# Kernel tuning notes

Measured on AMD Instinct MI355X. Metric: run time of the kernel, lower is better.

The kernel has to match this reference:

```python
import jax, jax.numpy as jnp
import numpy as np

B, S, D, H = 2, 2048, 2048, 16
HD = D // H  # 128


def setup_inputs() -> dict:
    key = jax.random.key(0)
    ks = jax.random.split(key, 5)
    scale = 0.02
    return {
        "hidden_states": jax.random.normal(ks[0], (B, S, D), dtype=jnp.float32),
        "Wqkv_w": jax.random.normal(ks[1], (3 * D, D), dtype=jnp.float32) * scale,
        "Wqkv_b": jax.random.normal(ks[2], (3 * D,), dtype=jnp.float32) * scale,
        "out_w": jax.random.normal(ks[3], (D, D), dtype=jnp.float32) * scale,
        "out_b": jax.random.normal(ks[4], (D,), dtype=jnp.float32) * scale,
    }


def reference(hidden_states, Wqkv_w, Wqkv_b, out_w, out_b):
    b, s, d = hidden_states.shape
    # QKV projection (torch Linear: x @ W.T + b)
    qkv = hidden_states @ Wqkv_w.T + Wqkv_b          # [b, s, 3d]
    qkv = qkv.reshape(b, s, 3, H, HD)                 # 'b s (three h d)'
    q, k, v = qkv[:, :, 0], qkv[:, :, 1], qkv[:, :, 2]  # [b, s, h, hd]
    softmax_scale = 1.0 / np.float32(np.sqrt(HD))
    # full quadratic scores, matching the naive baddbmm path
    scores = jnp.einsum('bthd,bshd->bhts', q, k) * softmax_scale  # [b,h,t,s]
    # causal=False (module default), dropout_p=0.0 -> no mask, no dropout
    attn = jax.nn.softmax(scores, axis=-1)
    ctx = jnp.einsum('bhts,bshd->bthd', attn, v)      # [b, t, h, hd]
    ctx = ctx.reshape(b, s, d)
    return ctx @ out_w.T + out_b
```

## Files before the change

### kernel.cpp

```cpp
#include <hip/hip_runtime.h>
#include <cstdint>
#include <cstddef>

#define B_ 2
#define S_ 2048
#define D_ 2048
#define H_ 16
#define HD_ 128
#define NTOK 4096
#define NQKV 6144

typedef unsigned short u16;
typedef __attribute__((ext_vector_type(8))) __bf16 bf16x8;
typedef __attribute__((ext_vector_type(4))) float f32x4;

__device__ __forceinline__ u16 f2bf(float f) {
  uint32_t u = __builtin_bit_cast(uint32_t, f);
  u = (u + 0x7FFFu + ((u >> 16) & 1u)) >> 16;
  return (u16)u;
}

__device__ __forceinline__ void gload_lds16(const void* g, void* l) {
  __builtin_amdgcn_global_load_lds(
      (const __attribute__((address_space(1))) void*)g,
      (__attribute__((address_space(3))) void*)l, 16, 0, 0);
}

__global__ void cvt_all(const float* __restrict__ hs, const float* __restrict__ wqkv,
                        const float* __restrict__ wo,
                        u16* __restrict__ hsb, u16* __restrict__ wqkvb,
                        u16* __restrict__ wob) {
  const int n1 = (B_ * S_ * D_) / 8;
  const int n2 = n1 + (NQKV * D_) / 8;
  const int n3 = n2 + (D_ * D_) / 8;
  int idx = blockIdx.x * blockDim.x + threadIdx.x;
  int stride = gridDim.x * blockDim.x;
  for (int i = idx; i < n3; i += stride) {
    const float* src; u16* dst; int j;
    if (i < n1)      { src = hs;   dst = hsb;   j = i; }
    else if (i < n2) { src = wqkv; dst = wqkvb; j = i - n1; }
    else             { src = wo;   dst = wob;   j = i - n2; }
    const float4* s = (const float4*)(src + (size_t)j * 8);
    float4 a = s[0], b = s[1];
    union { u16 u[8]; uint4 v; } o;
    o.u[0] = f2bf(a.x); o.u[1] = f2bf(a.y); o.u[2] = f2bf(a.z); o.u[3] = f2bf(a.w);
    o.u[4] = f2bf(b.x); o.u[5] = f2bf(b.y); o.u[6] = f2bf(b.z); o.u[7] = f2bf(b.w);
    *(uint4*)(dst + (size_t)j * 8) = o.v;
  }
}


#define PH_MID() do { asm volatile("s_barrier" ::: "memory"); \
  __builtin_amdgcn_s_setprio(1); } while (0)
#define PH_END() do { __builtin_amdgcn_s_setprio(0); \
  asm volatile("s_barrier" ::: "memory"); } while (0)
#define PH_END_VM(n) do { __builtin_amdgcn_s_setprio(0); \
  asm volatile("s_waitcnt vmcnt(" #n ")" ::: "memory"); \
  asm volatile("s_barrier" ::: "memory"); } while (0)

#define STA(sl,buf,ko) gload_lds16(aSrc + (size_t)(sl)*64*D_ + (ko), aDst + (buf)*16384 + (sl)*4096)
#define STB(sl,buf,ko) gload_lds16(bSrc + (size_t)(sl)*64*D_ + (ko), bDst + (buf)*12288 + (sl)*4096)

#define LOADB(buf) do { _Pragma("unroll") for (int nf = 0; nf < 3; ++nf) \
  _Pragma("unroll") for (int kk = 0; kk < 2; ++kk) \
    breg[nf][kk] = *(const bf16x8*)(sB + (buf)*12288 + (wn*48 + nf*16 + fr)*64 + ((((kk<<2)|fq)^swz)<<3)); } while (0)
#define LOADA_A(buf,q) do { _Pragma("unroll") for (int mm = 0; mm < 2; ++mm) \
  _Pragma("unroll") for (int kk = 0; kk < 2; ++kk) \
    arA[mm][kk] = *(const bf16x8*)(sA + (buf)*16384 + (wm*128 + ((q)*2+mm)*16 + fr)*64 + ((((kk<<2)|fq)^swz)<<3)); } while (0)
#define LOADA_B(buf,q) do { _Pragma("unroll") for (int mm = 0; mm < 2; ++mm) \
  _Pragma("unroll") for (int kk = 0; kk < 2; ++kk) \
    arB[mm][kk] = *(const bf16x8*)(sA + (buf)*16384 + (wm*128 + ((q)*2+mm)*16 + fr)*64 + ((((kk<<2)|fq)^swz)<<3)); } while (0)
#define MFMA12_A(q) do { _Pragma("unroll") for (int kk = 0; kk < 2; ++kk) \
  _Pragma("unroll") for (int mm = 0; mm < 2; ++mm) \
  _Pragma("unroll") for (int nf = 0; nf < 3; ++nf) \
    acc[(q)*2+mm][nf] = __builtin_amdgcn_mfma_f32_16x16x32_bf16(arA[mm][kk], breg[nf][kk], acc[(q)*2+mm][nf], 0, 0, 0); } while (0)
#define MFMA12_B(q) do { _Pragma("unroll") for (int kk = 0; kk < 2; ++kk) \
  _Pragma("unroll") for (int mm = 0; mm < 2; ++mm) \
  _Pragma("unroll") for (int nf = 0; nf < 3; ++nf) \
    acc[(q)*2+mm][nf] = __builtin_amdgcn_mfma_f32_16x16x32_bf16(arB[mm][kk], breg[nf][kk], acc[(q)*2+mm][nf], 0, 0, 0); } while (0)

__global__ __launch_bounds__(512, 2) void qkv_gemm(
    const u16* __restrict__ hsb, const u16* __restrict__ wb,
    const float* __restrict__ bias,
    u16* __restrict__ qb, u16* __restrict__ kb, u16* __restrict__ vT)
{
  __shared__ alignas(1024) u16 sA[2 * 16384];
  __shared__ alignas(1024) u16 sB[2 * 12288];
  const int tid = threadIdx.x;
  const int lane = tid & 63, wid = tid >> 6;
  const int wm = wid >> 2, wn = wid & 3;
  const int fr = lane & 15, fq = lane >> 4;
  const int swz = fr & 7;
  const int m0 = blockIdx.x * 256, n0 = blockIdx.y * 192;

  const int r8 = tid >> 3, g8 = (tid & 7) ^ (r8 & 7);
  const u16* aSrc = hsb + (size_t)(m0 + r8) * D_ + g8 * 8;
  const u16* bSrc = wb  + (size_t)(n0 + r8) * D_ + g8 * 8;
  u16* aDst = sA + wid * 512;
  u16* bDst = sB + wid * 512;

  f32x4 acc[8][3];
  f32x4 z = {0.f, 0.f, 0.f, 0.f};
#pragma unroll
  for (int m = 0; m < 8; ++m)
#pragma unroll
    for (int n = 0; n < 3; ++n) acc[m][n] = z;

  bf16x8 breg[3][2], arA[2][2], arB[2][2];

  STB(0,0,0); STB(1,0,0); STB(2,0,0); STA(0,0,0); STA(1,0,0); STA(2,0,0); STA(3,0,0);
  STB(0,1,64); STB(1,1,64); STB(2,1,64); STA(0,1,64); STA(2,1,64);
  asm volatile("s_waitcnt vmcnt(5)" ::: "memory");
  asm volatile("s_barrier" ::: "memory");

  const int NI = D_ / 128;
#pragma unroll 1
  for (int j = 0; j < NI - 1; ++j) {
    const int kS = (2*j + 1) * 64;
    const int kA = (2*j + 2) * 64;
    const int kB = (2*j + 3) * 64;
    LOADB(0); LOADA_A(0,0); LOADA_B(0,1); STA(1,1,kS); STA(3,1,kS); PH_MID(); MFMA12_A(0); PH_END();
    LOADA_A(0,2);                         STB(0,0,kA); STB(1,0,kA); PH_MID(); MFMA12_B(1); PH_END();
    LOADA_B(0,3);                         STB(2,0,kA); STA(0,0,kA); PH_MID(); MFMA12_A(2); PH_END();
                                          STA(2,0,kA);              PH_MID(); MFMA12_B(3); PH_END_VM(5);
    LOADB(1); LOADA_A(1,0); LOADA_B(1,1); STA(1,0,kA); STA(3,0,kA); PH_MID(); MFMA12_A(0); PH_END();
    LOADA_A(1,2);                         STB(0,1,kB); STB(1,1,kB); PH_MID(); MFMA12_B(1); PH_END();
    LOADA_B(1,3);                         STB(2,1,kB); STA(0,1,kB); PH_MID(); MFMA12_A(2); PH_END();
                                          STA(2,1,kB);              PH_MID(); MFMA12_B(3); PH_END_VM(5);
  }
  {
    const int kS = (2*NI - 1) * 64;
    LOADB(0); LOADA_A(0,0); LOADA_B(0,1); STA(1,1,kS); STA(3,1,kS); PH_MID(); MFMA12_A(0); PH_END();
    LOADA_A(0,2);                                                   PH_MID(); MFMA12_B(1); PH_END();
    LOADA_B(0,3);                                                   PH_MID(); MFMA12_A(2); PH_END();
                                                                    PH_MID(); MFMA12_B(3); PH_END_VM(0);
    LOADB(1); LOADA_A(1,0); LOADA_B(1,1);                           PH_MID(); MFMA12_A(0); PH_END();
    LOADA_A(1,2);                                                   PH_MID(); MFMA12_B(1); PH_END();
    LOADA_B(1,3);                                                   PH_MID(); MFMA12_A(2); PH_END();
                                                                    PH_MID(); MFMA12_B(3); PH_END();
  }

  const float qscale = 0.08838834764831845f;
#pragma unroll
  for (int mf = 0; mf < 8; ++mf)
#pragma unroll
    for (int nf = 0; nf < 3; ++nf) {
      int col = n0 + wn * 48 + nf * 16 + fr;
      float bv = bias[col];
      int t = col >> 11;
      int d2 = col & 2047;
      int h = d2 >> 7, hd = d2 & 127;
#pragma unroll
      for (int r = 0; r < 4; ++r) {
        int row = m0 + wm * 128 + mf * 16 + fq * 4 + r;
        int bb = row >> 11, s = row & 2047;
        int bh = bb * H_ + h;
        float val = acc[mf][nf][r] + bv;
        if (t == 0)      qb[((size_t)bh * S_ + s) * HD_ + hd] = f2bf(val * qscale);
        else if (t == 1) kb[((size_t)bh * S_ + s) * HD_ + hd] = f2bf(val);
        else             vT[((size_t)bh * HD_ + hd) * S_ + s] = f2bf(val);
      }
    }
}

__device__ __forceinline__ void gemm_bt_tile(
    const u16* __restrict__ A, const u16* __restrict__ B,
    int lda, int ldb, int K, int m0, int n0,
    u16* As, u16* Bs, f32x4 acc[4][4])
{
  const int tid = threadIdx.x;
  const int lane = tid & 63;
  const int wid = tid >> 6;
  const int wr = wid >> 1, wc = wid & 1;
  const int fr = lane & 15, fq = lane >> 4;

  for (int k0 = 0; k0 < K; k0 += 32) {
    __syncthreads();
#pragma unroll
    for (int i = 0; i < 2; ++i) {
      int cbase = (i * 4 + wid) * 64;
      int c = cbase + lane;
      int r = c >> 2, c8 = (c & 3) * 8;
      gload_lds16(A + (size_t)(m0 + r) * lda + k0 + c8, As + (size_t)cbase * 8);
      gload_lds16(B + (size_t)(n0 + r) * ldb + k0 + c8, Bs + (size_t)cbase * 8);
    }
    __syncthreads();

    bf16x8 a[4], b[4];
#pragma unroll
    for (int m = 0; m < 4; ++m)
      a[m] = *(const bf16x8*)&As[(wr * 64 + m * 16 + fr) * 32 + fq * 8];
#pragma unroll
    for (int n = 0; n < 4; ++n)
      b[n] = *(const bf16x8*)&Bs[(wc * 64 + n * 16 + fr) * 32 + fq * 8];
#pragma unroll
    for (int m = 0; m < 4; ++m)
#pragma unroll
      for (int n = 0; n < 4; ++n)
        acc[m][n] = __builtin_amdgcn_mfma_f32_16x16x32_bf16(a[m], b[n], acc[m][n], 0, 0, 0);
  }
}

__global__ __launch_bounds__(256) void out_gemm(
    const u16* __restrict__ ctx, const u16* __restrict__ wo,
    const float* __restrict__ bias, float* __restrict__ out)
{
  __shared__ alignas(16) u16 As[128 * 32];
  __shared__ alignas(16) u16 Bs[128 * 32];
  f32x4 acc[4][4];
  f32x4 z = {0.f, 0.f, 0.f, 0.f};
#pragma unroll
  for (int m = 0; m < 4; ++m)
#pragma unroll
    for (int n = 0; n < 4; ++n) acc[m][n] = z;

  int m0 = blockIdx.x * 128, n0 = blockIdx.y * 128;
  gemm_bt_tile(ctx, wo, D_, D_, D_, m0, n0, As, Bs, acc);

  const int lane = threadIdx.x & 63;
  const int wid = threadIdx.x >> 6;
  const int wr = wid >> 1, wc = wid & 1;
  const int fr = lane & 15, fq = lane >> 4;
#pragma unroll
  for (int m = 0; m < 4; ++m)
#pragma unroll
    for (int n = 0; n < 4; ++n) {
      int col = n0 + wc * 64 + n * 16 + fr;
      float bv = bias[col];
#pragma unroll
      for (int r = 0; r < 4; ++r) {
        int row = m0 + wr * 64 + m * 16 + fq * 4 + r;
        out[(size_t)row * D_ + col] = acc[m][n][r] + bv;
      }
    }
}

#define STAGEKV(kvv, buf) do { _Pragma("unroll") \
  for (int i = 0; i < 4; ++i) { \
    int lk = i * 256 + tid; int rk = lk >> 4, sk = lk & 15; \
    gload_lds16(Kg + (size_t)((kvv) + rk) * HD_ + ((sk ^ (rk & 7)) << 3), \
                &Kl[buf][i * 2048 + wid * 512]); \
    int rv = lk >> 3, sv = lk & 7; \
    gload_lds16(Vg + (size_t)rv * S_ + (kvv) + ((sv ^ (rv & 7)) << 3), \
                &Vl[buf][i * 2048 + wid * 512]); \
  } } while (0)

__global__ __launch_bounds__(256, 2) void attn(
    const u16* __restrict__ qb, const u16* __restrict__ kb,
    const u16* __restrict__ vT, u16* __restrict__ ctx)
{
  __shared__ alignas(1024) u16 Kl[2][64 * 128];
  __shared__ alignas(1024) u16 Vl[2][128 * 64];
  __shared__ alignas(16) u16 Pl[4][32 * 64];

  const int tid = threadIdx.x, lane = tid & 63, wid = tid >> 6;
  const int fr = lane & 15, fq = lane >> 4;
  const int bh = blockIdx.y;
  const int q0 = blockIdx.x * 128 + wid * 32;
  f32x4 z = {0.f, 0.f, 0.f, 0.f};

  const u16* Kg = kb + (size_t)bh * S_ * HD_;
  const u16* Vg = vT + (size_t)bh * HD_ * S_;

  STAGEKV(0, 0);

  const u16* qbase = qb + ((size_t)bh * S_ + q0) * HD_;
  bf16x8 qa[2][4];
#pragma unroll
  for (int h = 0; h < 2; ++h)
#pragma unroll
    for (int kc = 0; kc < 4; ++kc)
      qa[h][kc] = *(const bf16x8*)(qbase + (size_t)(h * 16 + fr) * HD_ + kc * 32 + fq * 8);

  f32x4 accv[2][8];
#pragma unroll
  for (int h = 0; h < 2; ++h)
#pragma unroll
    for (int n = 0; n < 8; ++n) accv[h][n] = z;
  float m_run[2] = {-1e30f, -1e30f};
  float l_run[2] = {0.f, 0.f};

  __syncthreads();
  int cur = 0;

  for (int kv = 0; kv < S_; kv += 64) {
    if (kv + 64 < S_) STAGEKV(kv + 64, cur ^ 1);

    const u16* Kc = Kl[cur];
    const u16* Vc = Vl[cur];

    f32x4 sc[2][4];
    __builtin_amdgcn_s_setprio(1);
#pragma unroll
    for (int j = 0; j < 4; ++j) {
      f32x4 s0 = z, s1 = z;
#pragma unroll
      for (int kc = 0; kc < 4; ++kc) {
        int row = j * 16 + fr;
        bf16x8 kf = *(const bf16x8*)&Kc[row * 128 + ((kc * 32 + fq * 8) ^ ((row & 7) << 3))];
        s0 = __builtin_amdgcn_mfma_f32_16x16x32_bf16(kf, qa[0][kc], s0, 0, 0, 0);
        s1 = __builtin_amdgcn_mfma_f32_16x16x32_bf16(kf, qa[1][kc], s1, 0, 0, 0);
      }
      sc[0][j] = s0; sc[1][j] = s1;
    }
    __builtin_amdgcn_s_setprio(0);

    float pmax[2];
#pragma unroll
    for (int h = 0; h < 2; ++h) {
      float mx = sc[h][0][0];
#pragma unroll
      for (int j = 0; j < 4; ++j)
#pragma unroll
        for (int r = 0; r < 4; ++r) mx = fmaxf(mx, sc[h][j][r]);
      mx = fmaxf(mx, __shfl_xor(mx, 16));
      mx = fmaxf(mx, __shfl_xor(mx, 32));
      pmax[h] = mx;
    }

    int need = (pmax[0] > m_run[0] + 8.f) || (pmax[1] > m_run[1] + 8.f);
    if (__any(need)) {
#pragma unroll
      for (int h = 0; h < 2; ++h) {
        float mn = fmaxf(m_run[h], pmax[h]);
        float corr = __expf(m_run[h] - mn);
        m_run[h] = mn;
        l_run[h] *= corr;
#pragma unroll
        for (int r = 0; r < 4; ++r) {
          float rc = __shfl(corr, (lane & 48) | (fq * 4 + r));
#pragma unroll
          for (int n = 0; n < 8; ++n) accv[h][n][r] *= rc;
        }
      }
    }

    u16* Pw = Pl[wid];
#pragma unroll
    for (int h = 0; h < 2; ++h) {
      float ls = 0.f;
#pragma unroll
      for (int j = 0; j < 4; ++j) {
        union { u16 u[4]; ushort4 v; } pk;
#pragma unroll
        for (int r = 0; r < 4; ++r) {
          float p = __expf(sc[h][j][r] - m_run[h]);
          ls += p;
          pk.u[r] = f2bf(p);
        }
        int prow = h * 16 + fr;
        *(ushort4*)&Pw[prow * 64 + ((j * 16 + fq * 4) ^ ((fr & 7) << 3))] = pk.v;
      }
      ls += __shfl_xor(ls, 16);
      ls += __shfl_xor(ls, 32);
      l_run[h] += ls;
    }

    __builtin_amdgcn_s_setprio(1);
#pragma unroll
    for (int kc = 0; kc < 2; ++kc) {
      int pcol = (kc * 32 + fq * 8) ^ ((fr & 7) << 3);
      bf16x8 pa0 = *(const bf16x8*)&Pw[fr * 64 + pcol];
      bf16x8 pa1 = *(const bf16x8*)&Pw[(16 + fr) * 64 + pcol];
#pragma unroll
      for (int n = 0; n < 8; ++n) {
        int row = n * 16 + fr;
        bf16x8 vf = *(const bf16x8*)&Vc[row * 64 + ((kc * 32 + fq * 8) ^ ((row & 7) << 3))];
        accv[0][n] = __builtin_amdgcn_mfma_f32_16x16x32_bf16(pa0, vf, accv[0][n], 0, 0, 0);
        accv[1][n] = __builtin_amdgcn_mfma_f32_16x16x32_bf16(pa1, vf, accv[1][n], 0, 0, 0);
      }
    }
    __builtin_amdgcn_s_setprio(0);

    __syncthreads();
    cur ^= 1;
  }

  float inv[2][4];
#pragma unroll
  for (int h = 0; h < 2; ++h)
#pragma unroll
    for (int r = 0; r < 4; ++r) {
      float l = __shfl(l_run[h], (lane & 48) | (fq * 4 + r));
      inv[h][r] = 1.f / l;
    }
  u16* cb = ctx + (((size_t)(bh >> 4)) * S_ + q0) * D_ + (size_t)(bh & 15) * HD_;
#pragma unroll
  for (int h = 0; h < 2; ++h)
#pragma unroll
    for (int n = 0; n < 8; ++n)
#pragma unroll
      for (int r = 0; r < 4; ++r) {
        int q = h * 16 + fq * 4 + r;
        cb[(size_t)q * D_ + n * 16 + fr] = f2bf(accv[h][n][r] * inv[h][r]);
      }
}

extern "C" void kernel_launch(void* const* d_in, const int* in_sizes, int n_in,
                              void* d_out, int out_size, void* d_ws, size_t ws_size,
                              hipStream_t stream) {
  const float* hs   = (const float*)d_in[0];
  const float* wqkv = (const float*)d_in[1];
  const float* bqkv = (const float*)d_in[2];
  const float* wo   = (const float*)d_in[3];
  const float* bo   = (const float*)d_in[4];
  float* out = (float*)d_out;

  char* ws = (char*)d_ws;
  u16* hsb   = (u16*)(ws);
  u16* wqkvb = (u16*)(ws + 16777216);
  u16* wob   = (u16*)(ws + 41943040);
  u16* qb    = (u16*)(ws + 50331648);
  u16* kb    = (u16*)(ws + 67108864);
  u16* vT    = (u16*)(ws + 83886080);
  u16* ctx   = (u16*)(ws + 100663296);

  cvt_all<<<2048, 256, 0, stream>>>(hs, wqkv, wo, hsb, wqkvb, wob);

  qkv_gemm<<<dim3(NTOK / 256, NQKV / 192), 512, 0, stream>>>(hsb, wqkvb, bqkv, qb, kb, vT);
  attn<<<dim3(S_ / 128, B_ * H_), 256, 0, stream>>>(qb, kb, vT, ctx);
  out_gemm<<<dim3(NTOK / 128, D_ / 128), 256, 0, stream>>>(ctx, wob, bo, out);
}
```

Baseline: 292.8 us.

## Halve QKV GEMM M-tile to 128 rows and restructure pipeline for higher occupancy

The QKV projection GEMM tile shrinks from 256x192 to 128x192. That halves A-tile LDS and the accumulator registers, doubles the grid and raises the launch-bounds occupancy hint from 2 to 4 blocks per CU. The software-pipelined K loop is rewritten to four phases per iteration with new prefetch ordering and waitcnt values. The intent is more blocks in flight and better CU coverage (32x32 = 1024 blocks instead of 512), at the cost of lower arithmetic intensity per loaded B tile and more global traffic.

```diff
diff --git a/kernel.cpp b/kernel.cpp
--- a/kernel.cpp
+++ b/kernel.cpp
@@ -58,7 +58,7 @@
   asm volatile("s_waitcnt vmcnt(" #n ")" ::: "memory"); \
   asm volatile("s_barrier" ::: "memory"); } while (0)
 
-#define STA(sl,buf,ko) gload_lds16(aSrc + (size_t)(sl)*64*D_ + (ko), aDst + (buf)*16384 + (sl)*4096)
+#define STA(sl,buf,ko) gload_lds16(aSrc + (size_t)(sl)*64*D_ + (ko), aDst + (buf)*8192  + (sl)*4096)
 #define STB(sl,buf,ko) gload_lds16(bSrc + (size_t)(sl)*64*D_ + (ko), bDst + (buf)*12288 + (sl)*4096)
 
 #define LOADB(buf) do { _Pragma("unroll") for (int nf = 0; nf < 3; ++nf) \
@@ -66,10 +66,10 @@
     breg[nf][kk] = *(const bf16x8*)(sB + (buf)*12288 + (wn*48 + nf*16 + fr)*64 + ((((kk<<2)|fq)^swz)<<3)); } while (0)
 #define LOADA_A(buf,q) do { _Pragma("unroll") for (int mm = 0; mm < 2; ++mm) \
   _Pragma("unroll") for (int kk = 0; kk < 2; ++kk) \
-    arA[mm][kk] = *(const bf16x8*)(sA + (buf)*16384 + (wm*128 + ((q)*2+mm)*16 + fr)*64 + ((((kk<<2)|fq)^swz)<<3)); } while (0)
+    arA[mm][kk] = *(const bf16x8*)(sA + (buf)*8192 + (wm*64 + ((q)*2+mm)*16 + fr)*64 + ((((kk<<2)|fq)^swz)<<3)); } while (0)
 #define LOADA_B(buf,q) do { _Pragma("unroll") for (int mm = 0; mm < 2; ++mm) \
   _Pragma("unroll") for (int kk = 0; kk < 2; ++kk) \
-    arB[mm][kk] = *(const bf16x8*)(sA + (buf)*16384 + (wm*128 + ((q)*2+mm)*16 + fr)*64 + ((((kk<<2)|fq)^swz)<<3)); } while (0)
+    arB[mm][kk] = *(const bf16x8*)(sA + (buf)*8192 + (wm*64 + ((q)*2+mm)*16 + fr)*64 + ((((kk<<2)|fq)^swz)<<3)); } while (0)
 #define MFMA12_A(q) do { _Pragma("unroll") for (int kk = 0; kk < 2; ++kk) \
   _Pragma("unroll") for (int mm = 0; mm < 2; ++mm) \
   _Pragma("unroll") for (int nf = 0; nf < 3; ++nf) \
@@ -79,19 +79,19 @@
   _Pragma("unroll") for (int nf = 0; nf < 3; ++nf) \
     acc[(q)*2+mm][nf] = __builtin_amdgcn_mfma_f32_16x16x32_bf16(arB[mm][kk], breg[nf][kk], acc[(q)*2+mm][nf], 0, 0, 0); } while (0)
 
-__global__ __launch_bounds__(512, 2) void qkv_gemm(
+__global__ __launch_bounds__(512, 4) void qkv_gemm(
     const u16* __restrict__ hsb, const u16* __restrict__ wb,
     const float* __restrict__ bias,
     u16* __restrict__ qb, u16* __restrict__ kb, u16* __restrict__ vT)
 {
-  __shared__ alignas(1024) u16 sA[2 * 16384];
+  __shared__ alignas(1024) u16 sA[2 * 8192];
   __shared__ alignas(1024) u16 sB[2 * 12288];
   const int tid = threadIdx.x;
   const int lane = tid & 63, wid = tid >> 6;
   const int wm = wid >> 2, wn = wid & 3;
   const int fr = lane & 15, fq = lane >> 4;
   const int swz = fr & 7;
-  const int m0 = blockIdx.x * 256, n0 = blockIdx.y * 192;
+  const int m0 = blockIdx.x * 128, n0 = blockIdx.y * 192;
 
   const int r8 = tid >> 3, g8 = (tid & 7) ^ (r8 & 7);
   const u16* aSrc = hsb + (size_t)(m0 + r8) * D_ + g8 * 8;
@@ -99,50 +99,47 @@
   u16* aDst = sA + wid * 512;
   u16* bDst = sB + wid * 512;
 
-  f32x4 acc[8][3];
+  f32x4 acc[4][3];
   f32x4 z = {0.f, 0.f, 0.f, 0.f};
 #pragma unroll
-  for (int m = 0; m < 8; ++m)
+  for (int m = 0; m < 4; ++m)
 #pragma unroll
     for (int n = 0; n < 3; ++n) acc[m][n] = z;
 
   bf16x8 breg[3][2], arA[2][2], arB[2][2];
 
-  STB(0,0,0); STB(1,0,0); STB(2,0,0); STA(0,0,0); STA(1,0,0); STA(2,0,0); STA(3,0,0);
-  STB(0,1,64); STB(1,1,64); STB(2,1,64); STA(0,1,64); STA(2,1,64);
-  asm volatile("s_waitcnt vmcnt(5)" ::: "memory");
+  STB(0,0,0); STB(1,0,0); STB(2,0,0); STA(0,0,0); STA(1,0,0);
+  STB(0,1,64); STB(1,1,64); STB(2,1,64);
+  asm volatile("s_waitcnt vmcnt(3)" ::: "memory");
   asm volatile("s_barrier" ::: "memory");
 
-  const int NI = D_ / 128;
 #pragma unroll 1
-  for (int j = 0; j < NI - 1; ++j) {
-    const int kS = (2*j + 1) * 64;
-    const int kA = (2*j + 2) * 64;
-    const int kB = (2*j + 3) * 64;
-    LOADB(0); LOADA_A(0,0); LOADA_B(0,1); STA(1,1,kS); STA(3,1,kS); PH_MID(); MFMA12_A(0); PH_END();
-    LOADA_A(0,2);                         STB(0,0,kA); STB(1,0,kA); PH_MID(); MFMA12_B(1); PH_END();
-    LOADA_B(0,3);                         STB(2,0,kA); STA(0,0,kA); PH_MID(); MFMA12_A(2); PH_END();
-                                          STA(2,0,kA);              PH_MID(); MFMA12_B(3); PH_END_VM(5);
-    LOADB(1); LOADA_A(1,0); LOADA_B(1,1); STA(1,0,kA); STA(3,0,kA); PH_MID(); MFMA12_A(0); PH_END();
-    LOADA_A(1,2);                         STB(0,1,kB); STB(1,1,kB); PH_MID(); MFMA12_B(1); PH_END();
-    LOADA_B(1,3);                         STB(2,1,kB); STA(0,1,kB); PH_MID(); MFMA12_A(2); PH_END();
-                                          STA(2,1,kB);              PH_MID(); MFMA12_B(3); PH_END_VM(5);
+  for (int j = 0; j < 15; ++j) {
+    const int kA1 = (2*j + 1) * 64;
+    const int kB2 = (2*j + 2) * 64;
+    const int kB3 = (2*j + 3) * 64;
+    LOADB(0); LOADA_A(0,0); LOADA_B(0,1); STA(0,1,kA1); STA(1,1,kA1);
+      PH_MID(); MFMA12_A(0); PH_END();
+    STB(0,0,kB2); STB(1,0,kB2); STB(2,0,kB2);
+      PH_MID(); MFMA12_B(1); PH_END_VM(3);
+    LOADB(1); LOADA_A(1,0); LOADA_B(1,1); STA(0,0,kB2); STA(1,0,kB2);
+      PH_MID(); MFMA12_A(0); PH_END();
+    STB(0,1,kB3); STB(1,1,kB3); STB(2,1,kB3);
+      PH_MID(); MFMA12_B(1); PH_END_VM(3);
   }
   {
-    const int kS = (2*NI - 1) * 64;
-    LOADB(0); LOADA_A(0,0); LOADA_B(0,1); STA(1,1,kS); STA(3,1,kS); PH_MID(); MFMA12_A(0); PH_END();
-    LOADA_A(0,2);                                                   PH_MID(); MFMA12_B(1); PH_END();
-    LOADA_B(0,3);                                                   PH_MID(); MFMA12_A(2); PH_END();
-                                                                    PH_MID(); MFMA12_B(3); PH_END_VM(0);
-    LOADB(1); LOADA_A(1,0); LOADA_B(1,1);                           PH_MID(); MFMA12_A(0); PH_END();
-    LOADA_A(1,2);                                                   PH_MID(); MFMA12_B(1); PH_END();
-    LOADA_B(1,3);                                                   PH_MID(); MFMA12_A(2); PH_END();
-                                                                    PH_MID(); MFMA12_B(3); PH_END();
+    const int kA31 = 31 * 64;
+    LOADB(0); LOADA_A(0,0); LOADA_B(0,1); STA(0,1,kA31); STA(1,1,kA31);
+      PH_MID(); MFMA12_A(0); PH_END();
+      PH_MID(); MFMA12_B(1); PH_END_VM(0);
+    LOADB(1); LOADA_A(1,0); LOADA_B(1,1);
+      PH_MID(); MFMA12_A(0); PH_END();
+      PH_MID(); MFMA12_B(1); PH_END();
   }
 
   const float qscale = 0.08838834764831845f;
 #pragma unroll
-  for (int mf = 0; mf < 8; ++mf)
+  for (int mf = 0; mf < 4; ++mf)
 #pragma unroll
     for (int nf = 0; nf < 3; ++nf) {
       int col = n0 + wn * 48 + nf * 16 + fr;
@@ -152,7 +149,7 @@
       int h = d2 >> 7, hd = d2 & 127;
 #pragma unroll
       for (int r = 0; r < 4; ++r) {
-        int row = m0 + wm * 128 + mf * 16 + fq * 4 + r;
+        int row = m0 + wm * 64 + mf * 16 + fq * 4 + r;
         int bb = row >> 11, s = row & 2047;
         int bh = bb * H_ + h;
         float val = acc[mf][nf][r] + bv;
@@ -417,7 +414,7 @@
 
   cvt_all<<<2048, 256, 0, stream>>>(hs, wqkv, wo, hsb, wqkvb, wob);
 
-  qkv_gemm<<<dim3(NTOK / 256, NQKV / 192), 512, 0, stream>>>(hsb, wqkvb, bqkv, qb, kb, vT);
+  qkv_gemm<<<dim3(NTOK / 128, NQKV / 192), 512, 0, stream>>>(hsb, wqkvb, bqkv, qb, kb, vT);
   attn<<<dim3(S_ / 128, B_ * H_), 256, 0, stream>>>(qb, kb, vT, ctx);
   out_gemm<<<dim3(NTOK / 128, D_ / 128), 256, 0, stream>>>(ctx, wob, bo, out);
 }
```

Result: no change. 297.1 us (+1.5%).
